# Performance work log

Hardware: AMD Instinct MI355X
Metric: run time of the kernel (lower is better)

## Reference

```python
import jax, jax.numpy as jnp
import numpy as np

KW = 3          # kernel_width
PAD = (KW - 1) // 2


def setup_inputs() -> dict:
    key = jax.random.key(0)
    ks = jax.random.split(key, 7)
    B, Lq, Lk, D, C = 8, 1024, 1024, 512, 512  # D=q_size, C=k_size
    return {
        "q": jax.random.normal(ks[0], (B, Lq, D), jnp.float32),
        "k": jax.random.normal(ks[1], (B, Lk, C), jnp.float32),
        "W_kernel": jax.random.normal(ks[2], (D, C * KW), jnp.float32) * (1.0 / np.sqrt(D)),
        "b_kernel": jax.random.normal(ks[3], (C * KW,), jnp.float32) * 0.02,
        "W_bias": jax.random.normal(ks[4], (D, 1), jnp.float32) * (1.0 / np.sqrt(D)),
        "b_bias": jax.random.normal(ks[5], (1,), jnp.float32) * 0.02,
        "bias_b": jax.random.normal(ks[6], (1,), jnp.float32),
    }


def reference(q, k, W_kernel, b_kernel, W_bias, b_bias, bias_b):
    B, Lq, D = q.shape
    _, Lk, C = k.shape
    # per-(batch, query) dynamic conv kernels: [B, Lq, C, KW]
    kernel = (q @ W_kernel + b_kernel).reshape(B, Lq, C, KW)
    # per-(batch, query) scalar bias: [B, Lq]
    bias = (q @ W_bias + b_bias)[..., 0]
    # windowed view of k (cross-correlation with 'same' padding)
    kpad = jnp.pad(k, ((0, 0), (PAD, PAD), (0, 0)))  # [B, Lk+2*PAD, C]
    win_idx = jnp.arange(Lk)[:, None] + jnp.arange(KW)[None, :]  # [Lk, KW]
    kwin = kpad[:, win_idx, :]  # [B, Lk, KW, C]
    # a[b,i,j] = sum_{c,w} kernel[b,i,c,w] * kpad[b, j+w, c] + bias[b,i] + bias_b
    a_ij = jnp.einsum('bicw,bjwc->bij', kernel, kwin)
    return a_ij + bias[:, :, None] + bias_b
```

## Files before the change

### kernel.cpp

```cpp
#include <hip/hip_runtime.h>


typedef __attribute__((ext_vector_type(8))) short s8vec;
typedef __attribute__((ext_vector_type(4))) float floatx4;

__device__ __forceinline__ unsigned short f2bf(float f) {
    union { float f; unsigned u; } v; v.f = f;
    unsigned r = (v.u + 0x7FFFu + ((v.u >> 16) & 1u)) >> 16;
    return (unsigned short)r;
}

__device__ __forceinline__ void gl2lds16(const void* g, void* l) {
    __builtin_amdgcn_global_load_lds(
        (__attribute__((address_space(1))) void*)(g),
        (__attribute__((address_space(3))) void*)(l), 16, 0, 0);
}

__global__ void cvt_all(const float* __restrict__ q, const float* __restrict__ k,
                        unsigned short* __restrict__ qbf, unsigned short* __restrict__ kp) {
    int t = blockIdx.x * blockDim.x + threadIdx.x;
    if (t < 524288) {
        const float4* p = (const float4*)q + 2 * (size_t)t;
        float4 a = p[0], b = p[1];
        union { unsigned short s[8]; uint4 v; } o;
        o.s[0]=f2bf(a.x); o.s[1]=f2bf(a.y); o.s[2]=f2bf(a.z); o.s[3]=f2bf(a.w);
        o.s[4]=f2bf(b.x); o.s[5]=f2bf(b.y); o.s[6]=f2bf(b.z); o.s[7]=f2bf(b.w);
        ((uint4*)qbf)[t] = o.v;
    } else if (t < 1048576) {
        int e8 = t - 524288;
        size_t e = (size_t)e8 * 8;
        int b = e8 >> 16;
        int j = (e8 >> 6) & 1023;
        int c = (e8 & 63) * 8;
        const float4* p = (const float4*)(k + e);
        float4 a = p[0], bb = p[1];
        union { unsigned short s[8]; uint4 v; } o;
        o.s[0]=f2bf(a.x); o.s[1]=f2bf(a.y); o.s[2]=f2bf(a.z); o.s[3]=f2bf(a.w);
        o.s[4]=f2bf(bb.x); o.s[5]=f2bf(bb.y); o.s[6]=f2bf(bb.z); o.s[7]=f2bf(bb.w);
        *(uint4*)(kp + ((size_t)(b * 1028 + j + 1) * 512 + c)) = o.v;
    } else if (t < 1050624) {
        int z = t - 1048576;
        int b = z >> 8, r = (z >> 6) & 3, ch = z & 63;
        int row = r ? (1024 + r) : 0;
        *(uint4*)(kp + ((size_t)(b * 1028 + row) * 512 + ch * 8)) = make_uint4(0u,0u,0u,0u);
    }
}

__global__ void prep_Wt(const float* __restrict__ W, unsigned short* __restrict__ Wt) {
    __shared__ float lds[32][33];
    int cw0 = blockIdx.x * 32, d0 = blockIdx.y * 32;
    int tx = threadIdx.x, ty = threadIdx.y;
    lds[ty][tx] = W[(size_t)(d0 + ty) * 1536 + cw0 + tx];
    __syncthreads();
    int cw = cw0 + ty;
    int c = cw / 3, w = cw % 3;
    Wt[((size_t)(w * 512 + c)) * 512 + d0 + tx] = f2bf(lds[tx][ty]);
}

__global__ void bias_kernel(const float* __restrict__ q, const float* __restrict__ Wb,
                            const float* __restrict__ b_bias, float* __restrict__ biasb) {
    int row  = blockIdx.x * 4 + (threadIdx.x >> 6);
    int lane = threadIdx.x & 63;
    const float4* qr = (const float4*)(q + (size_t)row * 512) + lane * 2;
    const float4* wb = (const float4*)Wb + lane * 2;
    float4 a0 = qr[0], a1 = qr[1], b0 = wb[0], b1 = wb[1];
    float s = a0.x*b0.x + a0.y*b0.y + a0.z*b0.z + a0.w*b0.w
            + a1.x*b1.x + a1.y*b1.y + a1.z*b1.z + a1.w*b1.w;
    #pragma unroll
    for (int off = 32; off > 0; off >>= 1) s += __shfl_down(s, off);
    if (lane == 0) biasb[row] = s + b_bias[0];
}

__global__ __launch_bounds__(256) void gemm_A(const unsigned short* __restrict__ Abf,
                                              const unsigned short* __restrict__ Bbf,
                                              const float* __restrict__ b_kernel,
                                              unsigned short* __restrict__ G) {
    __shared__ unsigned short lds_a[128 * 32];
    __shared__ unsigned short lds_b[128 * 32];
    int g = blockIdx.x;
    int xcd = g & 7, slot = g >> 3;
    int n_blk = slot / 8;
    int i_blk = xcd * 8 + (slot & 7);
    int i0 = i_blk * 128;
    int n0 = n_blk * 128;
    int tid = threadIdx.x, wid = tid >> 6, lane = tid & 63;
    int wm = wid >> 1, wn = wid & 1;
    floatx4 acc[4][4] = {};

    for (int kk = 0; kk < 512; kk += 32) {
        #pragma unroll
        for (int s = 0; s < 2; ++s) {
            int t = wid * 2 + s;
            const unsigned short* ga = Abf + (size_t)(i0 + t * 16 + (lane >> 2)) * 512 + kk + (lane & 3) * 8;
            gl2lds16(ga, (char*)lds_a + t * 1024);
            const unsigned short* gb = Bbf + (size_t)(n0 + t * 16 + (lane >> 2)) * 512 + kk + (lane & 3) * 8;
            gl2lds16(gb, (char*)lds_b + t * 1024);
        }
        __syncthreads();
        int ra = lane & 15, q8 = (lane >> 4) * 8;
        s8vec af[4], bf_[4];
        #pragma unroll
        for (int mi = 0; mi < 4; mi++)
            af[mi] = *(const s8vec*)(lds_a + (wm * 64 + mi * 16 + ra) * 32 + q8);
        #pragma unroll
        for (int ni = 0; ni < 4; ni++)
            bf_[ni] = *(const s8vec*)(lds_b + (wn * 64 + ni * 16 + ra) * 32 + q8);
        #pragma unroll
        for (int mi = 0; mi < 4; mi++)
            #pragma unroll
            for (int ni = 0; ni < 4; ni++)
                acc[mi][ni] = __builtin_amdgcn_mfma_f32_16x16x32_bf16(af[mi], bf_[ni], acc[mi][ni], 0, 0, 0);
        __syncthreads();
    }

    int cl = lane & 15, qd = lane >> 4;
    #pragma unroll
    for (int mi = 0; mi < 4; mi++) {
        #pragma unroll
        for (int ni = 0; ni < 4; ni++) {
            int n_all = n0 + wn * 64 + ni * 16 + cl;
            int c = n_all & 511, w = n_all >> 9;
            float bk = b_kernel[c * 3 + w];
            #pragma unroll
            for (int r = 0; r < 4; r++) {
                int i_g = i0 + wm * 64 + mi * 16 + qd * 4 + r;
                int b = i_g >> 10, ii = i_g & 1023;
                G[((size_t)((b * 3 + w) * 1024 + ii)) * 512 + c] = f2bf(acc[mi][ni][r] + bk);
            }
        }
    }
}

__global__ __launch_bounds__(256) void gemm_B(const unsigned short* __restrict__ G,
                                              const unsigned short* __restrict__ kp,
                                              const float* __restrict__ biasb,
                                              const float* __restrict__ bias_b,
                                              float* __restrict__ out) {
    __shared__ unsigned short lds_a[3 * 64 * 32];
    __shared__ unsigned short lds_k[144 * 32];
    int g = blockIdx.x;
    int b = g & 7, slot = g >> 3;
    int j0 = (slot & 7) * 128;
    int i0 = (slot >> 3) * 64;
    int tid = threadIdx.x, wid = tid >> 6, lane = tid & 63;
    int wn = wid;
    floatx4 acc[4][2] = {};
    const unsigned short* Gb  = G  + (size_t)b * 3 * 1024 * 512;
    const unsigned short* kpb = kp + (size_t)b * 1028 * 512;
    float bb = bias_b[0];

    for (int kk = 0; kk < 512; kk += 32) {
        #pragma unroll
        for (int s = 0; s < 3; ++s) {
            int t = wid * 3 + s;
            int w = t >> 2, chunk = t & 3;
            const unsigned short* ga = Gb + (size_t)(w * 1024 + i0 + chunk * 16 + (lane >> 2)) * 512
                                          + kk + (lane & 3) * 8;
            gl2lds16(ga, (char*)lds_a + t * 1024);
        }
        #pragma unroll
        for (int s = 0; s < 3; ++s) {
            int t = s * 4 + wid;
            if (t < 9) {
                const unsigned short* gk = kpb + (size_t)(j0 + t * 16 + (lane >> 2)) * 512
                                               + kk + (lane & 3) * 8;
                gl2lds16(gk, (char*)lds_k + t * 1024);
            }
        }
        __syncthreads();
        int ra = lane & 15, q8 = (lane >> 4) * 8;
        #pragma unroll
        for (int w = 0; w < 3; ++w) {
            s8vec af[4], bfr[2];
            #pragma unroll
            for (int mi = 0; mi < 4; mi++)
                af[mi] = *(const s8vec*)(lds_a + (w * 64 + mi * 16 + ra) * 32 + q8);
            #pragma unroll
            for (int ni = 0; ni < 2; ni++) {
                int rr = wn * 32 + ni * 16 + ra + w;
                bfr[ni] = *(const s8vec*)(lds_k + rr * 32 + q8);
            }
            #pragma unroll
            for (int mi = 0; mi < 4; mi++)
                #pragma unroll
                for (int ni = 0; ni < 2; ni++)
                    acc[mi][ni] = __builtin_amdgcn_mfma_f32_16x16x32_bf16(af[mi], bfr[ni], acc[mi][ni], 0, 0, 0);
        }
        __syncthreads();
    }

    int cl = lane & 15, qd = lane >> 4;
    #pragma unroll
    for (int mi = 0; mi < 4; mi++) {
        #pragma unroll
        for (int r = 0; r < 4; r++) {
            int i_loc = mi * 16 + qd * 4 + r;
            float bv = biasb[b * 1024 + i0 + i_loc] + bb;
            #pragma unroll
            for (int ni = 0; ni < 2; ni++) {
                int j_loc = wn * 32 + ni * 16 + cl;
                out[((size_t)(b * 1024 + i0 + i_loc)) * 1024 + j0 + j_loc] = acc[mi][ni][r] + bv;
            }
        }
    }
}

extern "C" void kernel_launch(void* const* d_in, const int* in_sizes, int n_in,
                              void* d_out, int out_size, void* d_ws, size_t ws_size,
                              hipStream_t stream) {
    const float* q        = (const float*)d_in[0];
    const float* k        = (const float*)d_in[1];
    const float* W_kernel = (const float*)d_in[2];
    const float* b_kernel = (const float*)d_in[3];
    const float* W_bias   = (const float*)d_in[4];
    const float* b_bias   = (const float*)d_in[5];
    const float* bias_b   = (const float*)d_in[6];
    float* out = (float*)d_out;

    char* ws = (char*)d_ws;
    unsigned short* q_bf = (unsigned short*)(ws);
    unsigned short* kp   = (unsigned short*)(ws + 8388608);
    unsigned short* Wt   = (unsigned short*)(ws + 8388608 + 8421376 + 16384);
    unsigned short* G    = (unsigned short*)(ws + 8388608 + 8421376 + 16384 + 1572864);
    float*          bsb  = (float*)(ws + 8388608 + 8421376 + 16384 + 1572864 + 25165824);

    cvt_all<<<4104, 256, 0, stream>>>(q, k, q_bf, kp);
    prep_Wt<<<dim3(48, 16), dim3(32, 32), 0, stream>>>(W_kernel, Wt);
    bias_kernel<<<2048, 256, 0, stream>>>(q, W_bias, b_bias, bsb);
    gemm_A<<<768, 256, 0, stream>>>(q_bf, Wt, b_kernel, G);
    gemm_B<<<1024, 256, 0, stream>>>(G, kp, bsb, bias_b, out);
}
```

Measured before the change: 152.1 us.

## Fuse bias kernel into conversion and halve GEMM block sizes to two waves

The bias dot-product kernel is merged into the conversion kernel as extra blocks, removing one launch. gemm_A switches to 64x128 tiles with 128 threads and 1536 blocks. gemm_B keeps its tile but uses two waves, each computing 64x64, so more MFMAs run per LDS fragment load. The trade-off is fewer waves per block to hide latency and more accumulator registers per wave.

```diff
diff --git a/kernel.cpp b/kernel.cpp
--- a/kernel.cpp
+++ b/kernel.cpp
@@ -17,32 +17,48 @@
 }
 
 __global__ void cvt_all(const float* __restrict__ q, const float* __restrict__ k,
-                        unsigned short* __restrict__ qbf, unsigned short* __restrict__ kp) {
-    int t = blockIdx.x * blockDim.x + threadIdx.x;
-    if (t < 524288) {
-        const float4* p = (const float4*)q + 2 * (size_t)t;
-        float4 a = p[0], b = p[1];
-        union { unsigned short s[8]; uint4 v; } o;
-        o.s[0]=f2bf(a.x); o.s[1]=f2bf(a.y); o.s[2]=f2bf(a.z); o.s[3]=f2bf(a.w);
-        o.s[4]=f2bf(b.x); o.s[5]=f2bf(b.y); o.s[6]=f2bf(b.z); o.s[7]=f2bf(b.w);
-        ((uint4*)qbf)[t] = o.v;
-    } else if (t < 1048576) {
-        int e8 = t - 524288;
-        size_t e = (size_t)e8 * 8;
-        int b = e8 >> 16;
-        int j = (e8 >> 6) & 1023;
-        int c = (e8 & 63) * 8;
-        const float4* p = (const float4*)(k + e);
-        float4 a = p[0], bb = p[1];
-        union { unsigned short s[8]; uint4 v; } o;
-        o.s[0]=f2bf(a.x); o.s[1]=f2bf(a.y); o.s[2]=f2bf(a.z); o.s[3]=f2bf(a.w);
-        o.s[4]=f2bf(bb.x); o.s[5]=f2bf(bb.y); o.s[6]=f2bf(bb.z); o.s[7]=f2bf(bb.w);
-        *(uint4*)(kp + ((size_t)(b * 1028 + j + 1) * 512 + c)) = o.v;
-    } else if (t < 1050624) {
-        int z = t - 1048576;
-        int b = z >> 8, r = (z >> 6) & 3, ch = z & 63;
-        int row = r ? (1024 + r) : 0;
-        *(uint4*)(kp + ((size_t)(b * 1028 + row) * 512 + ch * 8)) = make_uint4(0u,0u,0u,0u);
+                        unsigned short* __restrict__ qbf, unsigned short* __restrict__ kp,
+                        const float* __restrict__ Wb, const float* __restrict__ b_bias,
+                        float* __restrict__ biasb) {
+    int blk = blockIdx.x;
+    if (blk < 4104) {
+        int t = blk * 256 + threadIdx.x;
+        if (t < 524288) {
+            const float4* p = (const float4*)q + 2 * (size_t)t;
+            float4 a = p[0], b = p[1];
+            union { unsigned short s[8]; uint4 v; } o;
+            o.s[0]=f2bf(a.x); o.s[1]=f2bf(a.y); o.s[2]=f2bf(a.z); o.s[3]=f2bf(a.w);
+            o.s[4]=f2bf(b.x); o.s[5]=f2bf(b.y); o.s[6]=f2bf(b.z); o.s[7]=f2bf(b.w);
+            ((uint4*)qbf)[t] = o.v;
+        } else if (t < 1048576) {
+            int e8 = t - 524288;
+            size_t e = (size_t)e8 * 8;
+            int b = e8 >> 16;
+            int j = (e8 >> 6) & 1023;
+            int c = (e8 & 63) * 8;
+            const float4* p = (const float4*)(k + e);
+            float4 a = p[0], bb = p[1];
+            union { unsigned short s[8]; uint4 v; } o;
+            o.s[0]=f2bf(a.x); o.s[1]=f2bf(a.y); o.s[2]=f2bf(a.z); o.s[3]=f2bf(a.w);
+            o.s[4]=f2bf(bb.x); o.s[5]=f2bf(bb.y); o.s[6]=f2bf(bb.z); o.s[7]=f2bf(bb.w);
+            *(uint4*)(kp + ((size_t)(b * 1028 + j + 1) * 512 + c)) = o.v;
+        } else if (t < 1050624) {
+            int z = t - 1048576;
+            int b = z >> 8, r = (z >> 6) & 3, ch = z & 63;
+            int row = r ? (1024 + r) : 0;
+            *(uint4*)(kp + ((size_t)(b * 1028 + row) * 512 + ch * 8)) = make_uint4(0u,0u,0u,0u);
+        }
+    } else {
+        int row  = (blk - 4104) * 4 + (threadIdx.x >> 6);
+        int lane = threadIdx.x & 63;
+        const float4* qr = (const float4*)(q + (size_t)row * 512) + lane * 2;
+        const float4* wb = (const float4*)Wb + lane * 2;
+        float4 a0 = qr[0], a1 = qr[1], b0 = wb[0], b1 = wb[1];
+        float s = a0.x*b0.x + a0.y*b0.y + a0.z*b0.z + a0.w*b0.w
+                + a1.x*b1.x + a1.y*b1.y + a1.z*b1.z + a1.w*b1.w;
+        #pragma unroll
+        for (int off = 32; off > 0; off >>= 1) s += __shfl_down(s, off);
+        if (lane == 0) biasb[row] = s + b_bias[0];
     }
 }
 
@@ -57,54 +73,42 @@
     Wt[((size_t)(w * 512 + c)) * 512 + d0 + tx] = f2bf(lds[tx][ty]);
 }
 
-__global__ void bias_kernel(const float* __restrict__ q, const float* __restrict__ Wb,
-                            const float* __restrict__ b_bias, float* __restrict__ biasb) {
-    int row  = blockIdx.x * 4 + (threadIdx.x >> 6);
-    int lane = threadIdx.x & 63;
-    const float4* qr = (const float4*)(q + (size_t)row * 512) + lane * 2;
-    const float4* wb = (const float4*)Wb + lane * 2;
-    float4 a0 = qr[0], a1 = qr[1], b0 = wb[0], b1 = wb[1];
-    float s = a0.x*b0.x + a0.y*b0.y + a0.z*b0.z + a0.w*b0.w
-            + a1.x*b1.x + a1.y*b1.y + a1.z*b1.z + a1.w*b1.w;
-    #pragma unroll
-    for (int off = 32; off > 0; off >>= 1) s += __shfl_down(s, off);
-    if (lane == 0) biasb[row] = s + b_bias[0];
-}
-
-__global__ __launch_bounds__(256) void gemm_A(const unsigned short* __restrict__ Abf,
+__global__ __launch_bounds__(128) void gemm_A(const unsigned short* __restrict__ Abf,
                                               const unsigned short* __restrict__ Bbf,
                                               const float* __restrict__ b_kernel,
                                               unsigned short* __restrict__ G) {
-    __shared__ unsigned short lds_a[128 * 32];
+    __shared__ unsigned short lds_a[64 * 32];
     __shared__ unsigned short lds_b[128 * 32];
     int g = blockIdx.x;
     int xcd = g & 7, slot = g >> 3;
-    int n_blk = slot / 8;
-    int i_blk = xcd * 8 + (slot & 7);
-    int i0 = i_blk * 128;
-    int n0 = n_blk * 128;
+    int i_blk = xcd * 16 + (slot & 15);
+    int n_blk = slot >> 4;
+    int i0 = i_blk * 64, n0 = n_blk * 128;
     int tid = threadIdx.x, wid = tid >> 6, lane = tid & 63;
-    int wm = wid >> 1, wn = wid & 1;
     floatx4 acc[4][4] = {};
 
     for (int kk = 0; kk < 512; kk += 32) {
         #pragma unroll
-        for (int s = 0; s < 2; ++s) {
-            int t = wid * 2 + s;
-            const unsigned short* ga = Abf + (size_t)(i0 + t * 16 + (lane >> 2)) * 512 + kk + (lane & 3) * 8;
-            gl2lds16(ga, (char*)lds_a + t * 1024);
-            const unsigned short* gb = Bbf + (size_t)(n0 + t * 16 + (lane >> 2)) * 512 + kk + (lane & 3) * 8;
-            gl2lds16(gb, (char*)lds_b + t * 1024);
+        for (int s = 0; s < 6; ++s) {
+            int t = s * 2 + wid;
+            if (t < 4) {
+                const unsigned short* ga = Abf + (size_t)(i0 + t * 16 + (lane >> 2)) * 512 + kk + (lane & 3) * 8;
+                gl2lds16(ga, (char*)lds_a + t * 1024);
+            } else {
+                int u = t - 4;
+                const unsigned short* gb = Bbf + (size_t)(n0 + u * 16 + (lane >> 2)) * 512 + kk + (lane & 3) * 8;
+                gl2lds16(gb, (char*)lds_b + u * 1024);
+            }
         }
         __syncthreads();
         int ra = lane & 15, q8 = (lane >> 4) * 8;
         s8vec af[4], bf_[4];
         #pragma unroll
         for (int mi = 0; mi < 4; mi++)
-            af[mi] = *(const s8vec*)(lds_a + (wm * 64 + mi * 16 + ra) * 32 + q8);
+            af[mi] = *(const s8vec*)(lds_a + (mi * 16 + ra) * 32 + q8);
         #pragma unroll
         for (int ni = 0; ni < 4; ni++)
-            bf_[ni] = *(const s8vec*)(lds_b + (wn * 64 + ni * 16 + ra) * 32 + q8);
+            bf_[ni] = *(const s8vec*)(lds_b + (wid * 64 + ni * 16 + ra) * 32 + q8);
         #pragma unroll
         for (int mi = 0; mi < 4; mi++)
             #pragma unroll
@@ -118,12 +122,12 @@
     for (int mi = 0; mi < 4; mi++) {
         #pragma unroll
         for (int ni = 0; ni < 4; ni++) {
-            int n_all = n0 + wn * 64 + ni * 16 + cl;
+            int n_all = n0 + wid * 64 + ni * 16 + cl;
             int c = n_all & 511, w = n_all >> 9;
             float bk = b_kernel[c * 3 + w];
             #pragma unroll
             for (int r = 0; r < 4; r++) {
-                int i_g = i0 + wm * 64 + mi * 16 + qd * 4 + r;
+                int i_g = i0 + mi * 16 + qd * 4 + r;
                 int b = i_g >> 10, ii = i_g & 1023;
                 G[((size_t)((b * 3 + w) * 1024 + ii)) * 512 + c] = f2bf(acc[mi][ni][r] + bk);
             }
@@ -131,7 +135,7 @@
     }
 }
 
-__global__ __launch_bounds__(256) void gemm_B(const unsigned short* __restrict__ G,
+__global__ __launch_bounds__(128) void gemm_B(const unsigned short* __restrict__ G,
                                               const unsigned short* __restrict__ kp,
                                               const float* __restrict__ biasb,
                                               const float* __restrict__ bias_b,
@@ -143,47 +147,46 @@
     int j0 = (slot & 7) * 128;
     int i0 = (slot >> 3) * 64;
     int tid = threadIdx.x, wid = tid >> 6, lane = tid & 63;
-    int wn = wid;
-    floatx4 acc[4][2] = {};
+    floatx4 acc[4][4] = {};
     const unsigned short* Gb  = G  + (size_t)b * 3 * 1024 * 512;
     const unsigned short* kpb = kp + (size_t)b * 1028 * 512;
     float bb = bias_b[0];
 
     for (int kk = 0; kk < 512; kk += 32) {
         #pragma unroll
-        for (int s = 0; s < 3; ++s) {
-            int t = wid * 3 + s;
-            int w = t >> 2, chunk = t & 3;
-            const unsigned short* ga = Gb + (size_t)(w * 1024 + i0 + chunk * 16 + (lane >> 2)) * 512
-                                          + kk + (lane & 3) * 8;
-            gl2lds16(ga, (char*)lds_a + t * 1024);
-        }
-        #pragma unroll
-        for (int s = 0; s < 3; ++s) {
-            int t = s * 4 + wid;
-            if (t < 9) {
-                const unsigned short* gk = kpb + (size_t)(j0 + t * 16 + (lane >> 2)) * 512
-                                               + kk + (lane & 3) * 8;
-                gl2lds16(gk, (char*)lds_k + t * 1024);
+        for (int s = 0; s < 11; ++s) {
+            int t = s * 2 + wid;
+            if (t < 21) {
+                if (t < 12) {
+                    int w = t >> 2, chunk = t & 3;
+                    const unsigned short* ga = Gb + (size_t)(w * 1024 + i0 + chunk * 16 + (lane >> 2)) * 512
+                                                  + kk + (lane & 3) * 8;
+                    gl2lds16(ga, (char*)lds_a + t * 1024);
+                } else {
+                    int u = t - 12;
+                    const unsigned short* gk = kpb + (size_t)(j0 + u * 16 + (lane >> 2)) * 512
+                                                   + kk + (lane & 3) * 8;
+                    gl2lds16(gk, (char*)lds_k + u * 1024);
+                }
             }
         }
         __syncthreads();
         int ra = lane & 15, q8 = (lane >> 4) * 8;
         #pragma unroll
         for (int w = 0; w < 3; ++w) {
-            s8vec af[4], bfr[2];
+            s8vec af[4], bfr[4];
             #pragma unroll
             for (int mi = 0; mi < 4; mi++)
                 af[mi] = *(const s8vec*)(lds_a + (w * 64 + mi * 16 + ra) * 32 + q8);
             #pragma unroll
-            for (int ni = 0; ni < 2; ni++) {
-                int rr = wn * 32 + ni * 16 + ra + w;
+            for (int ni = 0; ni < 4; ni++) {
+                int rr = wid * 64 + ni * 16 + ra + w;
                 bfr[ni] = *(const s8vec*)(lds_k + rr * 32 + q8);
             }
             #pragma unroll
             for (int mi = 0; mi < 4; mi++)
                 #pragma unroll
-                for (int ni = 0; ni < 2; ni++)
+                for (int ni = 0; ni < 4; ni++)
                     acc[mi][ni] = __builtin_amdgcn_mfma_f32_16x16x32_bf16(af[mi], bfr[ni], acc[mi][ni], 0, 0, 0);
         }
         __syncthreads();
@@ -197,8 +200,8 @@
             int i_loc = mi * 16 + qd * 4 + r;
             float bv = biasb[b * 1024 + i0 + i_loc] + bb;
             #pragma unroll
-            for (int ni = 0; ni < 2; ni++) {
-                int j_loc = wn * 32 + ni * 16 + cl;
+            for (int ni = 0; ni < 4; ni++) {
+                int j_loc = wid * 64 + ni * 16 + cl;
                 out[((size_t)(b * 1024 + i0 + i_loc)) * 1024 + j0 + j_loc] = acc[mi][ni][r] + bv;
             }
         }
@@ -224,9 +227,8 @@
     unsigned short* G    = (unsigned short*)(ws + 8388608 + 8421376 + 16384 + 1572864);
     float*          bsb  = (float*)(ws + 8388608 + 8421376 + 16384 + 1572864 + 25165824);
 
-    cvt_all<<<4104, 256, 0, stream>>>(q, k, q_bf, kp);
+    cvt_all<<<6152, 256, 0, stream>>>(q, k, q_bf, kp, W_bias, b_bias, bsb);
     prep_Wt<<<dim3(48, 16), dim3(32, 32), 0, stream>>>(W_kernel, Wt);
-    bias_kernel<<<2048, 256, 0, stream>>>(q, W_bias, b_bias, bsb);
-    gemm_A<<<768, 256, 0, stream>>>(q_bf, Wt, b_kernel, G);
-    gemm_B<<<1024, 256, 0, stream>>>(G, kp, bsb, bias_b, out);
-}
+    gemm_A<<<1536, 128, 0, stream>>>(q_bf, Wt, b_kernel, G);
+    gemm_B<<<1024, 128, 0, stream>>>(G, kp, bsb, bias_b, out);
+}
```

After: 152.0 us. No clear change (-0.0%).
